# Optimization experiments

Measured on AMD Instinct MI355X. Metric: run time of the kernel, lower is better.

## Reference

```python
import jax, jax.numpy as jnp
import numpy as np

B = 8192          # batch
DIM = 2048        # feature dim
FANOUT = 10       # balanced 10-ary tree, depth 3 -> 1000 leaves
N_NODES = 1 + 10 + 100  # inner nodes with classifiers = 111
NUM_CLASSES = 1000


def setup_inputs() -> dict:
    key = jax.random.key(0)
    k1, k2, k3, k4 = jax.random.split(key, 4)
    x = jax.random.normal(k1, (B, DIM), dtype=jnp.float32)
    labels = jax.random.randint(k2, (B,), 0, NUM_CLASSES, dtype=jnp.int64 if jax.config.jax_enable_x64 else jnp.int32)
    # Stacked per-node Linear(dim, num_child+1): column 0 is the extra slot
    # included in the softmax but never routed to (children use cols 1..FANOUT).
    W = jax.random.normal(k3, (N_NODES, DIM, FANOUT + 1), dtype=jnp.float32) * (1.0 / np.sqrt(DIM))
    b = jax.random.normal(k4, (N_NODES, FANOUT + 1), dtype=jnp.float32) * 0.01
    return {"x": x, "labels": labels, "W": W, "b": b}


def reference(x, labels, W, b):
    # All 111 tiny per-node Linear+softmax classifiers fused into one batched GEMM.
    logits = jnp.einsum('bd,ndk->bnk', x, W) + b          # [B, 111, 11]
    probs = jax.nn.softmax(logits, axis=-1)               # softmax over num_child+1 (incl. dummy col 0)
    # Hierarchical path probabilities (root.path_prob = 1.0):
    # level-1 nodes are children of root (node 0), via softmax columns 1..10.
    p1 = probs[:, 0, 1:]                                   # [B, 10]
    # level-2 nodes: children of nodes 1..10
    p2 = (p1[:, :, None] * probs[:, 1:11, 1:]).reshape(x.shape[0], 100)    # [B, 100]
    # leaves: children of nodes 11..110 -> 1000 classes (out[:, 1:] slice already applied)
    out = (p2[:, :, None] * probs[:, 11:111, 1:]).reshape(x.shape[0], NUM_CLASSES)  # [B, 1000]
    penalty = jnp.float32(0.0)
    return (out, penalty)
```

## Files before the change

kernel.cpp:

```cpp
#include <hip/hip_runtime.h>
#include <hip/hip_bf16.h>
#include <hip/hip_fp16.h>

typedef _Float16 f16;
typedef __attribute__((ext_vector_type(8))) _Float16 f16x8;
typedef __attribute__((ext_vector_type(4))) float f32x4;

#define DIM     2048
#define BROWS   8192
#define NCOLS   1221
#define NPAD    1280
#define NNODES  111
#define BM      128
#define BN      128
#define BK      32
#define NKT     (DIM / BK)
#define MT      (BROWS / BM)
#define NT      (NPAD / BN)

__global__ __launch_bounds__(256) void prep_x(const float* __restrict__ X,
                                              f16* __restrict__ Xf) {
    __shared__ float T[128 * 68];
    int blk = blockIdx.x;
    int mt = blk >> 5, kt = blk & 31;
    int t = threadIdx.x;
    int row = t >> 1, half = t & 1;
    const float* src = X + (size_t)(mt * 128 + row) * DIM + kt * 64 + half * 32;
    float* dst = T + row * 68 + half * 32;
    #pragma unroll
    for (int i = 0; i < 8; ++i) ((f32x4*)dst)[i] = ((const f32x4*)src)[i];
    __syncthreads();
    int w = t >> 6, l = t & 63, r = l & 15, q = l >> 4;
    f16* out = Xf + (size_t)blk * 8192;
    #pragma unroll
    for (int p = 0; p < 4; ++p) {
        int gk = p * 4 + w;
        int kk = gk >> 3, g = gk & 7;
        const float* s = T + (g * 16 + r) * 68 + kk * 32 + q * 8;
        f32x4 a = *(const f32x4*)s;
        f32x4 b = *(const f32x4*)(s + 4);
        f16x8 h;
        h[0] = (f16)a[0]; h[1] = (f16)a[1]; h[2] = (f16)a[2]; h[3] = (f16)a[3];
        h[4] = (f16)b[0]; h[5] = (f16)b[1]; h[6] = (f16)b[2]; h[7] = (f16)b[3];
        *(f16x8*)(out + (size_t)(p * 256 + t) * 8) = h;
    }
}

__global__ void prep_b(const float* __restrict__ W, f16* __restrict__ Bf) {
    int idx = blockIdx.x * 256 + threadIdx.x;
    int c = idx & 1023, img = idx >> 10;
    int nt = img >> 5, kt = img & 31;
    int kk = c >> 9, g = (c >> 6) & 7, l = c & 63, r = l & 15, q = l >> 4;
    int col = nt * 128 + g * 16 + r;
    int d0  = kt * 64 + kk * 32 + q * 8;
    f16x8 v;
    if (col < NCOLS) {
        int n = col / 11, k = col - n * 11;
        const float* src = W + ((size_t)n * DIM + d0) * 11 + k;
        #pragma unroll
        for (int e = 0; e < 8; ++e) v[e] = (f16)src[(size_t)e * 11];
    } else {
        #pragma unroll
        for (int e = 0; e < 8; ++e) v[e] = (f16)0.f;
    }
    *(f16x8*)(Bf + (size_t)idx * 8) = v;
}

__global__ __launch_bounds__(512) void gemm_f16(const f16* __restrict__ Xf,
                                                const f16* __restrict__ Bf,
                                                f16* __restrict__ Lh) {
    __shared__ __align__(16) f16 As[2][4096];
    __shared__ __align__(16) f16 Bs[2][4096];

    int bid = blockIdx.x;
    int swz = (bid & 7) * 80 + (bid >> 3);
    int mt = swz / 10, nt = swz - mt * 10;

    int t = threadIdx.x, w = t >> 6, l = t & 63, r = l & 15, q = l >> 4;
    int wm = w >> 2, wn = w & 3;

    const f16* abase = Xf + (size_t)mt * 262144 + (size_t)t * 8;
    const f16* bbase = Bf + (size_t)nt * 262144 + (size_t)t * 8;

    f32x4 acc[4][2];
    #pragma unroll
    for (int i = 0; i < 4; ++i)
        #pragma unroll
        for (int j = 0; j < 2; ++j) acc[i][j] = (f32x4)0.f;

#define STAGE(KT, C)                                                             \
    {                                                                            \
        __builtin_amdgcn_global_load_lds(                                        \
            (const __attribute__((address_space(1))) void*)(abase + (size_t)(KT) * 4096), \
            (__attribute__((address_space(3))) void*)(&As[C][w * 512]), 16, 0, 0);        \
        __builtin_amdgcn_global_load_lds(                                        \
            (const __attribute__((address_space(1))) void*)(bbase + (size_t)(KT) * 4096), \
            (__attribute__((address_space(3))) void*)(&Bs[C][w * 512]), 16, 0, 0);        \
    }

#define COMPUTE(C)                                                               \
    {                                                                            \
        f16x8 af[4], bfr[2];                                                     \
        _Pragma("unroll")                                                        \
        for (int m = 0; m < 4; ++m)                                              \
            af[m] = *(const f16x8*)(&As[C][((wm * 4 + m) * 64 + l) * 8]);        \
        _Pragma("unroll")                                                        \
        for (int n = 0; n < 2; ++n)                                              \
            bfr[n] = *(const f16x8*)(&Bs[C][((wn * 2 + n) * 64 + l) * 8]);       \
        _Pragma("unroll")                                                        \
        for (int m = 0; m < 4; ++m)                                              \
            _Pragma("unroll")                                                    \
            for (int n = 0; n < 2; ++n)                                          \
                acc[m][n] = __builtin_amdgcn_mfma_f32_16x16x32_f16(af[m], bfr[n], acc[m][n], 0, 0, 0); \
    }

    STAGE(0, 0)

    #pragma unroll 2
    for (int kt = 0; kt < NKT - 1; ++kt) {
        int cc = kt & 1, cn = cc ^ 1;
        STAGE(kt + 1, cn)
        asm volatile("s_waitcnt vmcnt(2)" ::: "memory");
        __builtin_amdgcn_s_barrier();
        asm volatile("" ::: "memory");
        COMPUTE(cc)
        asm volatile("s_waitcnt lgkmcnt(0)" ::: "memory");
        __builtin_amdgcn_s_barrier();
        asm volatile("" ::: "memory");
    }
    asm volatile("s_waitcnt vmcnt(0)" ::: "memory");
    __builtin_amdgcn_s_barrier();
    asm volatile("" ::: "memory");
    COMPUTE(1)

#undef STAGE
#undef COMPUTE

    #pragma unroll
    for (int m = 0; m < 4; ++m) {
        int row = mt * 128 + wm * 64 + m * 16 + q * 4;
        #pragma unroll
        for (int n = 0; n < 2; ++n) {
            int col = nt * 128 + wn * 32 + n * 16 + r;
            #pragma unroll
            for (int j = 0; j < 4; ++j)
                Lh[(size_t)(row + j) * NPAD + col] = (f16)acc[m][n][j];
        }
    }
}

__global__ void tree_epi(const f16* __restrict__ L, const float* __restrict__ bias,
                         float* __restrict__ out) {
    __shared__ float P[4][NNODES * 11];
    __shared__ f16 R[4][NPAD];
    int w = threadIdx.x >> 6, l = threadIdx.x & 63;
    int row = blockIdx.x * 4 + w;

    const f16x8* src = (const f16x8*)(L + (size_t)row * NPAD);
    f16x8* dst = (f16x8*)R[w];
    dst[l]      = src[l];
    dst[l + 64] = src[l + 64];
    if (l < 32) dst[l + 128] = src[l + 128];

    for (int n = l; n < NNODES; n += 64) {
        float v[11], mx = -1e30f;
        #pragma unroll
        for (int k = 0; k < 11; ++k) { v[k] = (float)R[w][n * 11 + k] + bias[n * 11 + k]; mx = fmaxf(mx, v[k]); }
        float s = 0.f;
        #pragma unroll
        for (int k = 0; k < 11; ++k) { v[k] = __expf(v[k] - mx); s += v[k]; }
        float inv = 1.f / s;
        #pragma unroll
        for (int k = 0; k < 11; ++k) P[w][n * 11 + k] = v[k] * inv;
    }
    __syncthreads();
    const float* Pw = P[w];
    for (int c = l; c < 1000; c += 64) {
        int i  = c / 100;
        int j  = (c % 100) / 10;
        int mm = c % 10;
        float p = Pw[1 + i] * Pw[(1 + i) * 11 + 1 + j] * Pw[(11 + 10 * i + j) * 11 + 1 + mm];
        out[(size_t)row * 1000 + c] = p;
    }
    if (row == 0 && threadIdx.x == 0) out[(size_t)BROWS * 1000] = 0.f;
}

extern "C" void kernel_launch(void* const* d_in, const int* in_sizes, int n_in,
                              void* d_out, int out_size, void* d_ws, size_t ws_size,
                              hipStream_t stream) {
    const float* x    = (const float*)d_in[0];
    const float* W    = (const float*)d_in[2];
    const float* bias = (const float*)d_in[3];
    float* out = (float*)d_out;

    f16* Xf = (f16*)d_ws;
    f16* Bf = (f16*)((char*)d_ws + 33554432);
    f16* Lh = (f16*)((char*)d_ws + 38797312);

    prep_x <<<MT * 32, 256, 0, stream>>>(x, Xf);
    prep_b <<<1280, 256, 0, stream>>>(W, Bf);
    gemm_f16<<<MT * NT, 512, 0, stream>>>(Xf, Bf, Lh);
    tree_epi<<<BROWS / 4, 256, 0, stream>>>(Lh, bias, out);
}
```

Measured before the change: 106.9 us.

## Enlarge GEMM tiles to 256x256 with BK=64 and 8x4 MFMA accumulators per wave

The f16 GEMM block tile grows from 128x128 to 256x256 and the K step from 32 to 64. Each wave now holds 8x4 accumulator fragments and each stage loads four image panels for A and four for B. The aim is more reuse per LDS and global load and fewer K-loop barriers. In exchange the grid drops to 160 blocks, which is under one wave of blocks on a 256-CU device, and register and LDS use (128KB double-buffered) rise sharply, which may limit occupancy.

```diff
diff --git a/kernel.cpp b/kernel.cpp
--- a/kernel.cpp
+++ b/kernel.cpp
@@ -11,27 +11,25 @@
 #define NCOLS   1221
 #define NPAD    1280
 #define NNODES  111
-#define BM      128
-#define BN      128
-#define BK      32
+#define BK      64
 #define NKT     (DIM / BK)
-#define MT      (BROWS / BM)
-#define NT      (NPAD / BN)
+#define IMG     8192
+#define PANEL   (32 * IMG)
 
 __global__ __launch_bounds__(256) void prep_x(const float* __restrict__ X,
                                               f16* __restrict__ Xf) {
     __shared__ float T[128 * 68];
     int blk = blockIdx.x;
-    int mt = blk >> 5, kt = blk & 31;
+    int mp = blk >> 5, kt = blk & 31;
     int t = threadIdx.x;
     int row = t >> 1, half = t & 1;
-    const float* src = X + (size_t)(mt * 128 + row) * DIM + kt * 64 + half * 32;
+    const float* src = X + (size_t)(mp * 128 + row) * DIM + kt * 64 + half * 32;
     float* dst = T + row * 68 + half * 32;
     #pragma unroll
     for (int i = 0; i < 8; ++i) ((f32x4*)dst)[i] = ((const f32x4*)src)[i];
     __syncthreads();
     int w = t >> 6, l = t & 63, r = l & 15, q = l >> 4;
-    f16* out = Xf + (size_t)blk * 8192;
+    f16* out = Xf + (size_t)blk * IMG;
     #pragma unroll
     for (int p = 0; p < 4; ++p) {
         int gk = p * 4 + w;
@@ -49,9 +47,9 @@
 __global__ void prep_b(const float* __restrict__ W, f16* __restrict__ Bf) {
     int idx = blockIdx.x * 256 + threadIdx.x;
     int c = idx & 1023, img = idx >> 10;
-    int nt = img >> 5, kt = img & 31;
+    int np = img >> 5, kt = img & 31;
     int kk = c >> 9, g = (c >> 6) & 7, l = c & 63, r = l & 15, q = l >> 4;
-    int col = nt * 128 + g * 16 + r;
+    int col = np * 128 + g * 16 + r;
     int d0  = kt * 64 + kk * 32 + q * 8;
     f16x8 v;
     if (col < NCOLS) {
@@ -66,82 +64,87 @@
     *(f16x8*)(Bf + (size_t)idx * 8) = v;
 }
 
-__global__ __launch_bounds__(512) void gemm_f16(const f16* __restrict__ Xf,
-                                                const f16* __restrict__ Bf,
-                                                f16* __restrict__ Lh) {
-    __shared__ __align__(16) f16 As[2][4096];
-    __shared__ __align__(16) f16 Bs[2][4096];
+__global__ __launch_bounds__(512, 2) void gemm_f16(const f16* __restrict__ Xf,
+                                                   const f16* __restrict__ Bf,
+                                                   f16* __restrict__ Lh) {
+    __shared__ __align__(16) f16 As[2][16384];
+    __shared__ __align__(16) f16 Bs[2][16384];
 
     int bid = blockIdx.x;
-    int swz = (bid & 7) * 80 + (bid >> 3);
-    int mt = swz / 10, nt = swz - mt * 10;
+    int swz = (bid & 7) * 20 + (bid >> 3);
+    int mt = swz / 5, nt = swz - mt * 5;
 
     int t = threadIdx.x, w = t >> 6, l = t & 63, r = l & 15, q = l >> 4;
     int wm = w >> 2, wn = w & 3;
 
-    const f16* abase = Xf + (size_t)mt * 262144 + (size_t)t * 8;
-    const f16* bbase = Bf + (size_t)nt * 262144 + (size_t)t * 8;
-
-    f32x4 acc[4][2];
-    #pragma unroll
-    for (int i = 0; i < 4; ++i)
-        #pragma unroll
-        for (int j = 0; j < 2; ++j) acc[i][j] = (f32x4)0.f;
-
-#define STAGE(KT, C)                                                             \
-    {                                                                            \
-        __builtin_amdgcn_global_load_lds(                                        \
-            (const __attribute__((address_space(1))) void*)(abase + (size_t)(KT) * 4096), \
-            (__attribute__((address_space(3))) void*)(&As[C][w * 512]), 16, 0, 0);        \
-        __builtin_amdgcn_global_load_lds(                                        \
-            (const __attribute__((address_space(1))) void*)(bbase + (size_t)(KT) * 4096), \
-            (__attribute__((address_space(3))) void*)(&Bs[C][w * 512]), 16, 0, 0);        \
-    }
-
-#define COMPUTE(C)                                                               \
-    {                                                                            \
-        f16x8 af[4], bfr[2];                                                     \
-        _Pragma("unroll")                                                        \
-        for (int m = 0; m < 4; ++m)                                              \
-            af[m] = *(const f16x8*)(&As[C][((wm * 4 + m) * 64 + l) * 8]);        \
-        _Pragma("unroll")                                                        \
-        for (int n = 0; n < 2; ++n)                                              \
-            bfr[n] = *(const f16x8*)(&Bs[C][((wn * 2 + n) * 64 + l) * 8]);       \
-        _Pragma("unroll")                                                        \
-        for (int m = 0; m < 4; ++m)                                              \
-            _Pragma("unroll")                                                    \
-            for (int n = 0; n < 2; ++n)                                          \
-                acc[m][n] = __builtin_amdgcn_mfma_f32_16x16x32_f16(af[m], bfr[n], acc[m][n], 0, 0, 0); \
+    const f16* abase = Xf + (size_t)(mt * 2) * PANEL + (size_t)t * 8;
+    const f16* bbase = Bf + (size_t)(nt * 2) * PANEL + (size_t)t * 8;
+
+    f32x4 acc[8][4];
+    #pragma unroll
+    for (int i = 0; i < 8; ++i)
+        #pragma unroll
+        for (int j = 0; j < 4; ++j) acc[i][j] = (f32x4)0.f;
+
+#define STAGE(KT, C)                                                              \
+    {                                                                             \
+        _Pragma("unroll")                                                         \
+        for (int p = 0; p < 4; ++p) {                                             \
+            __builtin_amdgcn_global_load_lds(                                     \
+                (const __attribute__((address_space(1))) void*)                   \
+                    (abase + (size_t)(p >> 1) * PANEL + (size_t)(KT) * IMG + (p & 1) * 4096), \
+                (__attribute__((address_space(3))) void*)(&As[C][p * 4096 + w * 512]), 16, 0, 0); \
+            __builtin_amdgcn_global_load_lds(                                     \
+                (const __attribute__((address_space(1))) void*)                   \
+                    (bbase + (size_t)(p >> 1) * PANEL + (size_t)(KT) * IMG + (p & 1) * 4096), \
+                (__attribute__((address_space(3))) void*)(&Bs[C][p * 4096 + w * 512]), 16, 0, 0); \
+        }                                                                         \
+    }
+
+#define COMPUTE(C)                                                                \
+    {                                                                             \
+        _Pragma("unroll")                                                         \
+        for (int kk = 0; kk < 2; ++kk) {                                          \
+            f16x8 af[8], bfr[4];                                                  \
+            _Pragma("unroll")                                                     \
+            for (int m = 0; m < 8; ++m)                                           \
+                af[m] = *(const f16x8*)(&As[C][wm * 8192 + ((kk * 8 + m) * 64 + l) * 8]); \
+            _Pragma("unroll")                                                     \
+            for (int n = 0; n < 4; ++n)                                           \
+                bfr[n] = *(const f16x8*)(&Bs[C][(wn >> 1) * 8192                  \
+                            + ((kk * 8 + (wn & 1) * 4 + n) * 64 + l) * 8]);       \
+            _Pragma("unroll")                                                     \
+            for (int m = 0; m < 8; ++m)                                           \
+                _Pragma("unroll")                                                 \
+                for (int n = 0; n < 4; ++n)                                       \
+                    acc[m][n] = __builtin_amdgcn_mfma_f32_16x16x32_f16(af[m], bfr[n], acc[m][n], 0, 0, 0); \
+        }                                                                         \
     }
 
     STAGE(0, 0)
 
-    #pragma unroll 2
     for (int kt = 0; kt < NKT - 1; ++kt) {
         int cc = kt & 1, cn = cc ^ 1;
         STAGE(kt + 1, cn)
-        asm volatile("s_waitcnt vmcnt(2)" ::: "memory");
+        asm volatile("s_waitcnt vmcnt(8)" ::: "memory");
         __builtin_amdgcn_s_barrier();
-        asm volatile("" ::: "memory");
         COMPUTE(cc)
         asm volatile("s_waitcnt lgkmcnt(0)" ::: "memory");
         __builtin_amdgcn_s_barrier();
-        asm volatile("" ::: "memory");
     }
     asm volatile("s_waitcnt vmcnt(0)" ::: "memory");
     __builtin_amdgcn_s_barrier();
-    asm volatile("" ::: "memory");
     COMPUTE(1)
 
 #undef STAGE
 #undef COMPUTE
 
     #pragma unroll
-    for (int m = 0; m < 4; ++m) {
-        int row = mt * 128 + wm * 64 + m * 16 + q * 4;
-        #pragma unroll
-        for (int n = 0; n < 2; ++n) {
-            int col = nt * 128 + wn * 32 + n * 16 + r;
+    for (int m = 0; m < 8; ++m) {
+        int row = mt * 256 + wm * 128 + m * 16 + q * 4;
+        #pragma unroll
+        for (int n = 0; n < 4; ++n) {
+            int col = nt * 256 + wn * 64 + n * 16 + r;
             #pragma unroll
             for (int j = 0; j < 4; ++j)
                 Lh[(size_t)(row + j) * NPAD + col] = (f16)acc[m][n][j];
@@ -197,8 +200,8 @@
     f16* Bf = (f16*)((char*)d_ws + 33554432);
     f16* Lh = (f16*)((char*)d_ws + 38797312);
 
-    prep_x <<<MT * 32, 256, 0, stream>>>(x, Xf);
+    prep_x <<<64 * 32, 256, 0, stream>>>(x, Xf);
     prep_b <<<1280, 256, 0, stream>>>(W, Bf);
-    gemm_f16<<<MT * NT, 512, 0, stream>>>(Xf, Bf, Lh);
+    gemm_f16<<<160, 512, 0, stream>>>(Xf, Bf, Lh);
     tree_epi<<<BROWS / 4, 256, 0, stream>>>(Lh, bias, out);
 }
```

Result: faster. 104.2 us (-2.5%).
